# Kernel tuning notes

Measured on AMD Instinct MI355X. Metric: run time of the kernel, lower is better.

The kernel has to match this reference:

```python
import jax, jax.numpy as jnp
import numpy as np

ROPE_THETA = 10000.0

def apply_rope(x, positions):
    # x: [b, h, s, d], positions: [s]
    d = x.shape[-1]
    inv_freq = ROPE_THETA ** (-jnp.arange(0, d, 2, dtype=jnp.float32) / d)  # [d/2]
    ang = positions.astype(jnp.float32)[:, None] * inv_freq[None, :]        # [s, d/2]
    cos = jnp.cos(ang)
    sin = jnp.sin(ang)
    x1 = x[..., 0::2]
    x2 = x[..., 1::2]
    r1 = x1 * cos - x2 * sin
    r2 = x1 * sin + x2 * cos
    # interleave back to [..., d]
    return jnp.stack([r1, r2], axis=-1).reshape(x.shape)

def setup_inputs() -> dict:
    key = jax.random.key(0)
    k1, k2, k3 = jax.random.split(key, 3)
    b, s, d_model = 4, 2048, 1024
    x = jax.random.normal(k1, (b, s, d_model), dtype=jnp.float32)
    wqkv = jax.random.normal(k2, (3 * d_model, d_model), dtype=jnp.float32) * (d_model ** -0.5)
    wo = jax.random.normal(k3, (d_model, d_model), dtype=jnp.float32) * (d_model ** -0.5)
    token_positions = jnp.arange(s, dtype=jnp.int64 if jax.config.jax_enable_x64 else jnp.int32)
    return {"x": x, "wqkv": wqkv, "wo": wo, "token_positions": token_positions}

def reference(x, wqkv, wo, token_positions):
    b, s, d_model = x.shape
    num_heads = 16
    d_head = d_model // num_heads
    # fused QKV projection (Linear: y = x @ W.T)
    qkv = jnp.einsum('bse,fe->bsf', x, wqkv)  # [b, s, 3*d_model]
    q, k, v = jnp.split(qkv, 3, axis=-1)
    def to_heads(t):
        return t.reshape(b, s, num_heads, d_head).transpose(0, 2, 1, 3)  # [b, h, s, d]
    q, k, v = to_heads(q), to_heads(k), to_heads(v)
    q = apply_rope(q, token_positions)
    k = apply_rope(k, token_positions)
    scores = jnp.einsum('bhqd,bhkd->bhqk', q, k) / jnp.sqrt(jnp.asarray(d_head, dtype=x.dtype))
    causal = jnp.tril(jnp.ones((s, s), dtype=bool))  # [s, s]
    scores = jnp.where(causal, scores, -jnp.inf)
    weights = jax.nn.softmax(scores, axis=-1)
    y = jnp.einsum('bhqk,bhkd->bhqd', weights, v)
    y = y.transpose(0, 2, 1, 3).reshape(b, s, d_model)
    return jnp.einsum('bse,fe->bsf', y, wo)
```

## Files before the change

### kernel.cpp

```cpp
#include <hip/hip_runtime.h>
#include <stdint.h>


typedef __attribute__((ext_vector_type(8))) short bf16x8;
typedef __attribute__((ext_vector_type(4))) float f32x4;
typedef __attribute__((ext_vector_type(8))) unsigned short u16x8;
typedef __attribute__((ext_vector_type(4))) unsigned short u16x4;

#define NB 4
#define NS 2048
#define NH 16
#define DH 64
#define DM 1024
#define BH (NB*NH)

static __device__ __forceinline__ unsigned short f2bf(float f){
  unsigned u = __builtin_bit_cast(unsigned, f);
  u += 0x7fffu + ((u >> 16) & 1u);
  return (unsigned short)(u >> 16);
}
static __device__ __forceinline__ float bf2f(unsigned short h){
  unsigned u = ((unsigned)h) << 16;
  return __builtin_bit_cast(float, u);
}
static __device__ __forceinline__ unsigned cvt_pk_bf16(float lo, float hi){
  unsigned r;
  asm("v_cvt_pk_bf16_f32 %0, %1, %2" : "=v"(r) : "v"(lo), "v"(hi));
  return r;
}
static __device__ __forceinline__ f32x4 mfma16(bf16x8 a, bf16x8 b, f32x4 c){
  return __builtin_amdgcn_mfma_f32_16x16x32_bf16(a, b, c, 0, 0, 0);
}
static __device__ __forceinline__ void gld_lds16(const void* g, void* l){
  __builtin_amdgcn_global_load_lds((const __attribute__((address_space(1))) unsigned int*)g,
                                   (__attribute__((address_space(3))) unsigned int*)l,
                                   16, 0, 0);
}

__global__ __launch_bounds__(256) void cvt_all(const float* __restrict__ x,
                                               const float* __restrict__ wqkv,
                                               const float* __restrict__ wo,
                                               unsigned short* __restrict__ xb,
                                               unsigned short* __restrict__ wqkvb,
                                               unsigned short* __restrict__ wob){
  int stride = gridDim.x * blockDim.x;
  for (int i = blockIdx.x * blockDim.x + threadIdx.x; i < 3145728; i += stride){
    const float* src; unsigned short* dst; int j;
    if (i < 2097152){ src = x; dst = xb; j = i; }
    else if (i < 2883584){ src = wqkv; dst = wqkvb; j = i - 2097152; }
    else { src = wo; dst = wob; j = i - 2883584; }
    f32x4 v = *(const f32x4*)(src + (size_t)j * 4);
    u16x4 o;
    o[0] = f2bf(v[0]); o[1] = f2bf(v[1]); o[2] = f2bf(v[2]); o[3] = f2bf(v[3]);
    *(u16x4*)(dst + (size_t)j * 4) = o;
  }
}

__global__ void rope_table(const int* __restrict__ pos,
                           float* __restrict__ ct, float* __restrict__ st){
  int t = blockIdx.x * 256 + threadIdx.x;
  int s = t >> 5, i = t & 31;
  float p = (float)pos[s];
  float freq = exp2f(-(float)(2 * i) * (13.287712379549449f / 64.f));
  float a = p * freq;
  ct[t] = cosf(a);
  st[t] = sinf(a);
}

template<int BM, int BN, int MF, int NFR, int EPI>
__global__ __launch_bounds__((BM/(MF*16))*(BN/(NFR*16))*64, 2)
void gemm_ring(const unsigned short* __restrict__ A,
               const unsigned short* __restrict__ Bm,
               void* __restrict__ out0, void* __restrict__ out1,
               void* __restrict__ out2,
               const float* __restrict__ ct, const float* __restrict__ st,
               int M, int N, int K){
  constexpr int WM = BM / (MF * 16);
  constexpr int WN = BN / (NFR * 16);
  constexpr int T  = WM * WN * 64;
  constexpr int LA = BM * 4 / T;
  constexpr int LB = BN * 4 / T;
  __shared__ __attribute__((aligned(16))) unsigned short As[4][BM * 32];
  __shared__ __attribute__((aligned(16))) unsigned short Bs[4][BN * 32];
  int tid = threadIdx.x;
  int w = tid >> 6, l = tid & 63;
  int lr = l & 15, lk = l >> 4;

  int o = blockIdx.y * gridDim.x + blockIdx.x;
  int xcd = o & 7, t8 = o >> 3;
  int mpx = gridDim.y >> 3;
  int by = xcd * mpx + t8 / gridDim.x;
  int bx = t8 % gridDim.x;
  int m0 = by * BM, n0 = bx * BN;
  int wr = (w / WN) * (MF * 16), wc = (w % WN) * (NFR * 16);

  const int nt = K >> 5;

  auto stage = [&](int t, int buf){
    int k0 = t * 32;
#pragma unroll
    for (int i = 0; i < LA; i++){
      int f = i * T + tid;
      int row = f >> 2, c = f & 3;
      int gc = (c ^ ((row >> 1) & 3)) * 8;
      gld_lds16(A + (size_t)(m0 + row) * K + k0 + gc, &As[buf][(i * T + w * 64) * 8]);
    }
#pragma unroll
    for (int i = 0; i < LB; i++){
      int f = i * T + tid;
      int row = f >> 2, c = f & 3;
      int gc = (c ^ ((row >> 1) & 3)) * 8;
      gld_lds16(Bm + (size_t)(n0 + row) * K + k0 + gc, &Bs[buf][(i * T + w * 64) * 8]);
    }
  };

  f32x4 zero = {0.f, 0.f, 0.f, 0.f};
  f32x4 acc[MF][NFR];
#pragma unroll
  for (int a = 0; a < MF; a++)
#pragma unroll
    for (int b = 0; b < NFR; b++) acc[a][b] = zero;

  stage(0, 0); stage(1, 1); stage(2, 2);
  asm volatile("s_waitcnt vmcnt(%0)" :: "i"(2 * (LA + LB)) : "memory");
  __builtin_amdgcn_sched_barrier(0);
  __builtin_amdgcn_s_barrier();
  __builtin_amdgcn_sched_barrier(0);

  for (int t = 0; t < nt; ++t){
    int buf = t & 3;
    bf16x8 af[MF], bfr[NFR];
#pragma unroll
    for (int mf = 0; mf < MF; mf++){
      int row = wr + mf * 16 + lr;
      af[mf] = *(const bf16x8*)&As[buf][row * 32 + ((lk ^ ((row >> 1) & 3)) * 8)];
    }
#pragma unroll
    for (int nf = 0; nf < NFR; nf++){
      int row = wc + nf * 16 + lr;
      bfr[nf] = *(const bf16x8*)&Bs[buf][row * 32 + ((lk ^ ((row >> 1) & 3)) * 8)];
    }
    if (t + 3 < nt) stage(t + 3, (t + 3) & 3);
    __builtin_amdgcn_s_setprio(1);
#pragma unroll
    for (int mf = 0; mf < MF; mf++)
#pragma unroll
      for (int nf = 0; nf < NFR; nf++)
        acc[mf][nf] = mfma16(af[mf], bfr[nf], acc[mf][nf]);
    __builtin_amdgcn_s_setprio(0);
    if (t + 3 < nt)      { asm volatile("s_waitcnt vmcnt(%0)" :: "i"(2 * (LA + LB)) : "memory"); }
    else if (t + 2 < nt) { asm volatile("s_waitcnt vmcnt(%0)" :: "i"(LA + LB) : "memory"); }
    else if (t + 1 < nt) { asm volatile("s_waitcnt vmcnt(0)" ::: "memory"); }
    __builtin_amdgcn_sched_barrier(0);
    __builtin_amdgcn_s_barrier();
    __builtin_amdgcn_sched_barrier(0);
  }

  if (EPI == 0){
    unsigned short* q  = (unsigned short*)out0;
    unsigned short* k  = (unsigned short*)out1;
    unsigned short* vt = (unsigned short*)out2;
#pragma unroll
    for (int mf = 0; mf < MF; mf++)
#pragma unroll
      for (int nf = 0; nf < NFR; nf++)
#pragma unroll
        for (int j = 0; j < 4; j++){
          int m = m0 + wr + mf * 16 + lk * 4 + j;
          int n = n0 + wc + nf * 16 + lr;
          int part = n >> 10, c = n & 1023;
          int h = c >> 6, dh = c & 63;
          int b = m >> 11, s = m & (NS - 1);
          float val = acc[mf][nf][j];
          float other = __shfl_xor(val, 1);
          if (part == 2){
            vt[((size_t)((b * NH + h) * DH + dh)) * NS + s] = f2bf(val);
          } else {
            int ti = s * 32 + (dh >> 1);
            float cc = ct[ti], sn = st[ti];
            float r = (dh & 1) ? (other * sn + val * cc)
                               : (val * cc - other * sn);
            size_t off = ((size_t)(b * NH + h) * NS + s) * DH + dh;
            ((part == 0) ? q : k)[off] = f2bf(r);
          }
        }
  } else {
    float* C = (float*)out0;
#pragma unroll
    for (int mf = 0; mf < MF; mf++)
#pragma unroll
      for (int nf = 0; nf < NFR; nf++)
#pragma unroll
        for (int j = 0; j < 4; j++){
          int m = m0 + wr + mf * 16 + lk * 4 + j;
          int n = n0 + wc + nf * 16 + lr;
          C[(size_t)m * N + n] = acc[mf][nf][j];
        }
  }
}

__global__ __launch_bounds__(256, 3) void fa_kernel(const unsigned short* __restrict__ qb_,
                                                    const unsigned short* __restrict__ kbuf,
                                                    const unsigned short* __restrict__ vtb,
                                                    unsigned short* __restrict__ yb){
  __shared__ __attribute__((aligned(16))) unsigned short Kl[2][4096];
  __shared__ __attribute__((aligned(16))) unsigned short Vl[2][4096];
  __shared__ __attribute__((aligned(16))) unsigned short Pl[4][32 * 76];
  int tid = threadIdx.x;
  int w = tid >> 6, l = tid & 63;
  int lr = l & 15, lk = l >> 4;
  int qb = 15 - blockIdx.y;
  int bh = blockIdx.x;
  int b = bh >> 4, h = bh & 15;
  int qr0 = qb * 128 + w * 32;
  const unsigned short* Q  = qb_  + (size_t)bh * NS * DH;
  const unsigned short* Kp = kbuf + (size_t)bh * NS * DH;
  const unsigned short* VT = vtb  + (size_t)bh * DH * NS;
  unsigned short* Pw = &Pl[w][0];

  int r8  = l >> 3;
  int swc = ((l & 7) ^ (r8 & 7)) * 8;

  auto stage = [&](int buf, int t){
    int kbase = t * 64;
    if (w < 2){
#pragma unroll
      for (int ii = 0; ii < 4; ii++){
        int i = w * 4 + ii;
        gld_lds16(Kp + (size_t)(kbase + i * 8 + r8) * DH + swc, &Kl[buf][i * 512]);
      }
    } else {
#pragma unroll
      for (int ii = 0; ii < 4; ii++){
        int i = (w - 2) * 4 + ii;
        gld_lds16(VT + (size_t)(i * 8 + r8) * NS + kbase + swc, &Vl[buf][i * 512]);
      }
    }
  };

  bf16x8 qf[2][2];
#pragma unroll
  for (int mf = 0; mf < 2; mf++)
#pragma unroll
    for (int ks = 0; ks < 2; ks++)
      qf[mf][ks] = *(const bf16x8*)(Q + (size_t)(qr0 + mf * 16 + lr) * DH + ks * 32 + lk * 8);

  f32x4 zero = {0.f, 0.f, 0.f, 0.f};
  f32x4 O[2][4];
  float lsum[2];
#pragma unroll
  for (int mf = 0; mf < 2; mf++){
#pragma unroll
    for (int nf = 0; nf < 4; nf++) O[mf][nf] = zero;
    lsum[mf] = 0.f;
  }

  const float SC = 0.18033688011112042f;
  const int ntile = 2 * qb + 2;

  stage(0, 0);
  __syncthreads();

  int cur = 0;
  for (int t = 0; t < ntile; ++t){
    int kbase = t * 64;
    if (t + 1 < ntile) stage(cur ^ 1, t + 1);

    if (kbase <= qr0 + 31){
      bf16x8 kf[4][2];
#pragma unroll
      for (int nf = 0; nf < 4; nf++){
        int row = nf * 16 + lr;
        int ro = row * 64, sw = (row & 7) << 3;
#pragma unroll
        for (int ks = 0; ks < 2; ks++)
          kf[nf][ks] = *(const bf16x8*)&Kl[cur][ro + ((ks * 32 + lk * 8) ^ sw)];
      }
      bf16x8 vf[2][4];
#pragma unroll
      for (int nfd = 0; nfd < 4; nfd++){
        int row = nfd * 16 + lr;
        int ro = row * 64, sw = (row & 7) << 3;
#pragma unroll
        for (int ks = 0; ks < 2; ks++)
          vf[ks][nfd] = *(const bf16x8*)&Vl[cur][ro + ((ks * 32 + lk * 8) ^ sw)];
      }

      f32x4 sa[2][4];
#pragma unroll
      for (int mf = 0; mf < 2; mf++)
#pragma unroll
        for (int nf = 0; nf < 4; nf++) sa[mf][nf] = zero;
#pragma unroll
      for (int nf = 0; nf < 4; nf++)
#pragma unroll
        for (int mf = 0; mf < 2; mf++){
          sa[mf][nf] = mfma16(kf[nf][0], qf[mf][0], sa[mf][nf]);
          sa[mf][nf] = mfma16(kf[nf][1], qf[mf][1], sa[mf][nf]);
        }

      bool domask = (kbase + 63 > qr0);

#pragma unroll
      for (int mf = 0; mf < 2; mf++){
        int qg = qr0 + mf * 16 + lr;
        float ls = 0.f;
#pragma unroll
        for (int nf = 0; nf < 4; nf++){
          float p4[4];
#pragma unroll
          for (int j = 0; j < 4; j++){
            float xx = __builtin_fmaf(sa[mf][nf][j], SC, -8.0f);
            if (domask){
              int kg = kbase + nf * 16 + lk * 4 + j;
              if (kg > qg) xx = -__builtin_inff();
            }
            float p = exp2f(xx);
            ls += p;
            p4[j] = p;
          }
          unsigned d0 = cvt_pk_bf16(p4[0], p4[1]);
          unsigned d1 = cvt_pk_bf16(p4[2], p4[3]);
          int base = (mf * 16 + lr) * 76 + nf * 16 + lk * 4;
          *(unsigned*)&Pw[base]     = d0;
          *(unsigned*)&Pw[base + 2] = d1;
        }
        lsum[mf] += ls;
      }

      bf16x8 pf[2][2];
#pragma unroll
      for (int mf = 0; mf < 2; mf++)
#pragma unroll
        for (int ks = 0; ks < 2; ks++)
          pf[mf][ks] = *(const bf16x8*)&Pw[(mf * 16 + lr) * 76 + ks * 32 + lk * 8];
#pragma unroll
      for (int ks = 0; ks < 2; ks++)
#pragma unroll
        for (int nfd = 0; nfd < 4; nfd++)
#pragma unroll
          for (int mf = 0; mf < 2; mf++)
            O[mf][nfd] = mfma16(pf[mf][ks], vf[ks][nfd], O[mf][nfd]);
    }

    __syncthreads();
    cur ^= 1;
  }

#pragma unroll
  for (int mf = 0; mf < 2; mf++){
    lsum[mf] += __shfl_xor(lsum[mf], 16);
    lsum[mf] += __shfl_xor(lsum[mf], 32);
  }
#pragma unroll
  for (int mf = 0; mf < 2; mf++)
#pragma unroll
    for (int j = 0; j < 4; j++){
      float s = __shfl(lsum[mf], lk * 4 + j);
      float inv = 1.0f / s;
      int srow = qr0 + mf * 16 + lk * 4 + j;
      unsigned short* yp = yb + ((size_t)(b * NS + srow)) * DM + h * DH;
#pragma unroll
      for (int nfd = 0; nfd < 4; nfd++)
        yp[nfd * 16 + lr] = f2bf(O[mf][nfd][j] * inv);
    }
}

extern "C" void kernel_launch(void* const* d_in, const int* in_sizes, int n_in,
                              void* d_out, int out_size, void* d_ws, size_t ws_size,
                              hipStream_t stream){
  const float* x    = (const float*)d_in[0];
  const float* wqkv = (const float*)d_in[1];
  const float* wo   = (const float*)d_in[2];
  const int*   pos  = (const int*)d_in[3];
  float* out = (float*)d_out;

  char* ws = (char*)d_ws;
  size_t off = 0;
  auto alloc = [&](size_t bytes) -> void* {
    void* p = ws + off;
    off += (bytes + 255) & ~(size_t)255;
    return p;
  };
  const size_t NE = (size_t)BH * NS * DH;
  unsigned short* xb    = (unsigned short*)alloc((size_t)8192 * 1024 * 2);
  unsigned short* wqkvb = (unsigned short*)alloc((size_t)3072 * 1024 * 2);
  unsigned short* wob   = (unsigned short*)alloc((size_t)1024 * 1024 * 2);
  unsigned short* q  = (unsigned short*)alloc(NE * 2);
  unsigned short* k  = (unsigned short*)alloc(NE * 2);
  unsigned short* vt = (unsigned short*)alloc(NE * 2);
  unsigned short* y  = (unsigned short*)alloc(NE * 2);
  float* ct = (float*)alloc((size_t)NS * 32 * 4);
  float* st = (float*)alloc((size_t)NS * 32 * 4);

  cvt_all<<<3072, 256, 0, stream>>>(x, wqkv, wo, xb, wqkvb, wob);
  rope_table<<<256, 256, 0, stream>>>(pos, ct, st);
  gemm_ring<128, 128, 4, 4, 0><<<dim3(24, 64), 256, 0, stream>>>(
      xb, wqkvb, q, k, vt, ct, st, 8192, 3072, 1024);
  fa_kernel<<<dim3(64, 16), 256, 0, stream>>>(q, k, vt, y);
  gemm_ring<128, 128, 4, 4, 1><<<dim3(8, 64), 256, 0, stream>>>(
      y, wob, out, nullptr, nullptr, nullptr, nullptr, 8192, 1024, 1024);
}
```

Baseline: 229.9 us.

## Enlarge attention query tile to 256 rows and drop GEMM XCD block remap

The flash-attention kernel now gives each wave 64 query rows (256 per block), so every staged K/V tile is reused across twice as many queries. The score MFMAs are restructured per query fragment, and V fragments are loaded inside the PV loop to limit register pressure. Query blocks are reordered so the heaviest blocks launch first, and the P scratch stride changes to 72 with 64-bit stores. The GEMM also drops its XCD-aware block swizzle in favour of direct blockIdx mapping, which may reduce L2 locality. In exchange, the larger tile means fewer blocks, more registers and lower occupancy (launch bounds 3 to 2), and coarser causal-masking waste.

```diff
diff --git a/kernel.cpp b/kernel.cpp
--- a/kernel.cpp
+++ b/kernel.cpp
@@ -85,13 +85,7 @@
   int tid = threadIdx.x;
   int w = tid >> 6, l = tid & 63;
   int lr = l & 15, lk = l >> 4;
-
-  int o = blockIdx.y * gridDim.x + blockIdx.x;
-  int xcd = o & 7, t8 = o >> 3;
-  int mpx = gridDim.y >> 3;
-  int by = xcd * mpx + t8 / gridDim.x;
-  int bx = t8 % gridDim.x;
-  int m0 = by * BM, n0 = bx * BN;
+  int m0 = blockIdx.y * BM, n0 = blockIdx.x * BN;
   int wr = (w / WN) * (MF * 16), wc = (w % WN) * (NFR * 16);
 
   const int nt = K >> 5;
@@ -199,20 +193,21 @@
   }
 }
 
-__global__ __launch_bounds__(256, 3) void fa_kernel(const unsigned short* __restrict__ qb_,
+__global__ __launch_bounds__(256, 2) void fa_kernel(const unsigned short* __restrict__ qb_,
                                                     const unsigned short* __restrict__ kbuf,
                                                     const unsigned short* __restrict__ vtb,
                                                     unsigned short* __restrict__ yb){
   __shared__ __attribute__((aligned(16))) unsigned short Kl[2][4096];
   __shared__ __attribute__((aligned(16))) unsigned short Vl[2][4096];
-  __shared__ __attribute__((aligned(16))) unsigned short Pl[4][32 * 76];
+  __shared__ __attribute__((aligned(16))) unsigned short Pl[4][64 * 72];
   int tid = threadIdx.x;
   int w = tid >> 6, l = tid & 63;
   int lr = l & 15, lk = l >> 4;
-  int qb = 15 - blockIdx.y;
+  int yb_ = blockIdx.y;
+  int qb = (yb_ < 4) ? (7 - yb_) : (yb_ - 4);
   int bh = blockIdx.x;
   int b = bh >> 4, h = bh & 15;
-  int qr0 = qb * 128 + w * 32;
+  int qr0 = qb * 256 + w * 64;
   const unsigned short* Q  = qb_  + (size_t)bh * NS * DH;
   const unsigned short* Kp = kbuf + (size_t)bh * NS * DH;
   const unsigned short* VT = vtb  + (size_t)bh * DH * NS;
@@ -238,25 +233,25 @@
     }
   };
 
-  bf16x8 qf[2][2];
-#pragma unroll
-  for (int mf = 0; mf < 2; mf++)
+  bf16x8 qf[4][2];
+#pragma unroll
+  for (int mf = 0; mf < 4; mf++)
 #pragma unroll
     for (int ks = 0; ks < 2; ks++)
       qf[mf][ks] = *(const bf16x8*)(Q + (size_t)(qr0 + mf * 16 + lr) * DH + ks * 32 + lk * 8);
 
   f32x4 zero = {0.f, 0.f, 0.f, 0.f};
-  f32x4 O[2][4];
-  float lsum[2];
-#pragma unroll
-  for (int mf = 0; mf < 2; mf++){
+  f32x4 O[4][4];
+  float lsum[4];
+#pragma unroll
+  for (int mf = 0; mf < 4; mf++){
 #pragma unroll
     for (int nf = 0; nf < 4; nf++) O[mf][nf] = zero;
     lsum[mf] = 0.f;
   }
 
   const float SC = 0.18033688011112042f;
-  const int ntile = 2 * qb + 2;
+  const int ntile = 4 * qb + 4;
 
   stage(0, 0);
   __syncthreads();
@@ -266,7 +261,7 @@
     int kbase = t * 64;
     if (t + 1 < ntile) stage(cur ^ 1, t + 1);
 
-    if (kbase <= qr0 + 31){
+    if (kbase <= qr0 + 63){
       bf16x8 kf[4][2];
 #pragma unroll
       for (int nf = 0; nf < 4; nf++){
@@ -276,33 +271,18 @@
         for (int ks = 0; ks < 2; ks++)
           kf[nf][ks] = *(const bf16x8*)&Kl[cur][ro + ((ks * 32 + lk * 8) ^ sw)];
       }
-      bf16x8 vf[2][4];
-#pragma unroll
-      for (int nfd = 0; nfd < 4; nfd++){
-        int row = nfd * 16 + lr;
-        int ro = row * 64, sw = (row & 7) << 3;
-#pragma unroll
-        for (int ks = 0; ks < 2; ks++)
-          vf[ks][nfd] = *(const bf16x8*)&Vl[cur][ro + ((ks * 32 + lk * 8) ^ sw)];
-      }
-
-      f32x4 sa[2][4];
-#pragma unroll
-      for (int mf = 0; mf < 2; mf++)
-#pragma unroll
-        for (int nf = 0; nf < 4; nf++) sa[mf][nf] = zero;
-#pragma unroll
-      for (int nf = 0; nf < 4; nf++)
-#pragma unroll
-        for (int mf = 0; mf < 2; mf++){
-          sa[mf][nf] = mfma16(kf[nf][0], qf[mf][0], sa[mf][nf]);
-          sa[mf][nf] = mfma16(kf[nf][1], qf[mf][1], sa[mf][nf]);
-        }
-
       bool domask = (kbase + 63 > qr0);
 
 #pragma unroll
-      for (int mf = 0; mf < 2; mf++){
+      for (int mf = 0; mf < 4; mf++){
+        f32x4 sa[4];
+#pragma unroll
+        for (int nf = 0; nf < 4; nf++) sa[nf] = zero;
+#pragma unroll
+        for (int nf = 0; nf < 4; nf++){
+          sa[nf] = mfma16(kf[nf][0], qf[mf][0], sa[nf]);
+          sa[nf] = mfma16(kf[nf][1], qf[mf][1], sa[nf]);
+        }
         int qg = qr0 + mf * 16 + lr;
         float ls = 0.f;
 #pragma unroll
@@ -310,7 +290,7 @@
           float p4[4];
 #pragma unroll
           for (int j = 0; j < 4; j++){
-            float xx = __builtin_fmaf(sa[mf][nf][j], SC, -8.0f);
+            float xx = __builtin_fmaf(sa[nf][j], SC, -8.0f);
             if (domask){
               int kg = kbase + nf * 16 + lk * 4 + j;
               if (kg > qg) xx = -__builtin_inff();
@@ -319,28 +299,31 @@
             ls += p;
             p4[j] = p;
           }
-          unsigned d0 = cvt_pk_bf16(p4[0], p4[1]);
-          unsigned d1 = cvt_pk_bf16(p4[2], p4[3]);
-          int base = (mf * 16 + lr) * 76 + nf * 16 + lk * 4;
-          *(unsigned*)&Pw[base]     = d0;
-          *(unsigned*)&Pw[base + 2] = d1;
+          uint2 dd;
+          dd.x = cvt_pk_bf16(p4[0], p4[1]);
+          dd.y = cvt_pk_bf16(p4[2], p4[3]);
+          *(uint2*)&Pw[(mf * 16 + lr) * 72 + nf * 16 + lk * 4] = dd;
         }
         lsum[mf] += ls;
       }
 
-      bf16x8 pf[2][2];
-#pragma unroll
-      for (int mf = 0; mf < 2; mf++)
+      bf16x8 pf[4][2];
+#pragma unroll
+      for (int mf = 0; mf < 4; mf++)
 #pragma unroll
         for (int ks = 0; ks < 2; ks++)
-          pf[mf][ks] = *(const bf16x8*)&Pw[(mf * 16 + lr) * 76 + ks * 32 + lk * 8];
+          pf[mf][ks] = *(const bf16x8*)&Pw[(mf * 16 + lr) * 72 + ks * 32 + lk * 8];
 #pragma unroll
       for (int ks = 0; ks < 2; ks++)
 #pragma unroll
-        for (int nfd = 0; nfd < 4; nfd++)
-#pragma unroll
-          for (int mf = 0; mf < 2; mf++)
-            O[mf][nfd] = mfma16(pf[mf][ks], vf[ks][nfd], O[mf][nfd]);
+        for (int nfd = 0; nfd < 4; nfd++){
+          int row = nfd * 16 + lr;
+          int ro = row * 64, sw = (row & 7) << 3;
+          bf16x8 vf = *(const bf16x8*)&Vl[cur][ro + ((ks * 32 + lk * 8) ^ sw)];
+#pragma unroll
+          for (int mf = 0; mf < 4; mf++)
+            O[mf][nfd] = mfma16(pf[mf][ks], vf, O[mf][nfd]);
+        }
     }
 
     __syncthreads();
@@ -348,12 +331,12 @@
   }
 
 #pragma unroll
-  for (int mf = 0; mf < 2; mf++){
+  for (int mf = 0; mf < 4; mf++){
     lsum[mf] += __shfl_xor(lsum[mf], 16);
     lsum[mf] += __shfl_xor(lsum[mf], 32);
   }
 #pragma unroll
-  for (int mf = 0; mf < 2; mf++)
+  for (int mf = 0; mf < 4; mf++)
 #pragma unroll
     for (int j = 0; j < 4; j++){
       float s = __shfl(lsum[mf], lk * 4 + j);
@@ -397,7 +380,7 @@
   rope_table<<<256, 256, 0, stream>>>(pos, ct, st);
   gemm_ring<128, 128, 4, 4, 0><<<dim3(24, 64), 256, 0, stream>>>(
       xb, wqkvb, q, k, vt, ct, st, 8192, 3072, 1024);
-  fa_kernel<<<dim3(64, 16), 256, 0, stream>>>(q, k, vt, y);
+  fa_kernel<<<dim3(64, 8), 256, 0, stream>>>(q, k, vt, y);
   gemm_ring<128, 128, 4, 4, 1><<<dim3(8, 64), 256, 0, stream>>>(
       y, wob, out, nullptr, nullptr, nullptr, nullptr, 8192, 1024, 1024);
 }
```

After: 238.1 us. 3.5% more time.
